# Optimization experiments

Measured on AMD Instinct MI355X. Metric: run time of the kernel, lower is better.

Reference implementation:

```python
import jax, jax.numpy as jnp
import numpy as np

N_HEADS = 16
THETA = 10000.0

def rotate_half(x):
    x1, x2 = jnp.split(x, 2, axis=-1)
    return jnp.concatenate((-x2, x1), axis=-1)

def setup_inputs() -> dict:
    key = jax.random.key(0)
    k1, k2, k3 = jax.random.split(key, 3)
    B, T, C = 4, 2048, 2048
    x = jax.random.normal(k1, (B, T, C), dtype=jnp.float32)
    # torch Linear weights: y = x @ W.T
    wqkv = jax.random.normal(k2, (3 * C, C), dtype=jnp.float32) * (1.0 / np.sqrt(C))
    w_out = jax.random.normal(k3, (C, C), dtype=jnp.float32) * (1.0 / np.sqrt(C))
    return {"x": x, "wqkv": wqkv, "w_out": w_out}

def reference(x, wqkv, w_out):
    B, T, C = x.shape
    H = N_HEADS
    hd = C // H
    scale = 1.0 / np.sqrt(hd)

    qkv = x @ wqkv.T                               # [B, T, 3C]
    q, k, v = jnp.split(qkv, 3, axis=-1)
    q = q.reshape(B, T, H, hd).transpose(0, 2, 1, 3)  # [B, H, T, hd]
    k = k.reshape(B, T, H, hd).transpose(0, 2, 1, 3)
    v = v.reshape(B, T, H, hd).transpose(0, 2, 1, 3)

    # rotary embedding (kv_len == T, no cache)
    inv_freq = 1.0 / (THETA ** (jnp.arange(0, hd, 2, dtype=jnp.float32) / hd))
    t = jnp.arange(T, dtype=jnp.float32)
    freqs = jnp.einsum("i,j->ij", t, inv_freq)     # [T, hd/2]
    emb = jnp.concatenate((freqs, freqs), axis=-1) # [T, hd]
    cos = jnp.cos(emb)[None, None, :, :]
    sin = jnp.sin(emb)[None, None, :, :]
    q = q * cos + rotate_half(q) * sin
    k = k * cos + rotate_half(k) * sin

    scores = jnp.einsum("bhqd,bhkd->bhqk", q, k) * scale
    causal = jnp.triu(jnp.ones((T, T), dtype=bool), k=1)
    scores = jnp.where(causal[None, None], -jnp.inf, scores)
    attn = jax.nn.softmax(scores, axis=-1)
    out = jnp.einsum("bhqk,bhkd->bhqd", attn, v)   # [B, H, T, hd]
    out = out.transpose(0, 2, 1, 3).reshape(B, T, C)
    output = out @ w_out.T
    return (output, k, v)
```

## Files before the change

### kernel.cpp

```cpp
#include <hip/hip_runtime.h>

#define B_ 4
#define T_ 2048
#define C_ 2048
#define H_ 16
#define HD_ 128
#define BT_ (B_*T_)
#define N3_ (3*C_)

typedef unsigned short u16;
typedef unsigned int u32;
using short8 = __attribute__((ext_vector_type(8))) short;
using f32x4  = __attribute__((ext_vector_type(4))) float;

__device__ __forceinline__ u16 f2bf(float f) {
  union { float f; u32 u; } v; v.f = f;
  u32 r = v.u + 0x7FFFu + ((v.u >> 16) & 1u);
  return (u16)(r >> 16);
}
__device__ __forceinline__ float bf2f(u16 u) {
  union { u32 u; float f; } v; v.u = ((u32)u) << 16;
  return v.f;
}
__device__ __forceinline__ void gload_lds16(const void* g, void* l) {
  __builtin_amdgcn_global_load_lds((const __attribute__((address_space(1))) void*)g,
                                   (__attribute__((address_space(3))) void*)l, 16, 0, 0);
}

__global__ __launch_bounds__(256) void cast_f2b_kernel(const float* __restrict__ in,
                                                       u16* __restrict__ out, int n4) {
  int i = blockIdx.x * 256 + threadIdx.x;
  if (i >= n4) return;
  float4 v = ((const float4*)in)[i];
  ushort4 o;
  o.x = f2bf(v.x); o.y = f2bf(v.y); o.z = f2bf(v.z); o.w = f2bf(v.w);
  ((ushort4*)out)[i] = o;
}

__global__ __launch_bounds__(256) void rope_table_kernel(float* __restrict__ cosb,
                                                         float* __restrict__ sinb) {
  int i = blockIdx.x * 256 + threadIdx.x;
  int t = i >> 6, d = i & 63;
  float inv = powf(10000.0f, -(float)d / 64.0f);
  float ang = (float)t * inv;
  cosb[i] = cosf(ang);
  sinb[i] = sinf(ang);
}

__global__ __launch_bounds__(256) void rope_apply_kernel(const u16* __restrict__ qkv,
    const float* __restrict__ cosb, const float* __restrict__ sinb,
    u16* __restrict__ qb, u16* __restrict__ kbb,
    float* __restrict__ kout, float* __restrict__ vout) {
  int gid = blockIdx.x * 256 + threadIdx.x;
  int d = gid & 63;
  int h = (gid >> 6) & 15;
  int t = (gid >> 10) & 2047;
  int b = gid >> 21;
  const u16* row = qkv + (size_t)(b * T_ + t) * N3_;
  int base = h * HD_ + d;
  const float SCALE = 0.08838834764831845f;
  float q0 = bf2f(row[base]);
  float q1 = bf2f(row[base + 64]);
  float k0 = bf2f(row[C_ + base]);
  float k1 = bf2f(row[C_ + base + 64]);
  float v0 = bf2f(row[2*C_ + base]);
  float v1 = bf2f(row[2*C_ + base + 64]);
  float c = cosb[t * 64 + d], s = sinb[t * 64 + d];
  size_t o = ((size_t)((b * H_ + h) * T_ + t)) * HD_ + d;
  qb[o]        = f2bf((q0 * c - q1 * s) * SCALE);
  qb[o + 64]   = f2bf((q1 * c + q0 * s) * SCALE);
  float kr0 = k0 * c - k1 * s;
  float kr1 = k1 * c + k0 * s;
  kout[o]      = kr0;
  kout[o + 64] = kr1;
  kbb[o]       = f2bf(kr0);
  kbb[o + 64]  = f2bf(kr1);
  vout[o]      = v0;
  vout[o + 64] = v1;
}

__global__ __launch_bounds__(256) void vt_kernel(const u16* __restrict__ qkvb,
                                                 u16* __restrict__ vtb) {
  __shared__ u16 tile[64][72];
  int bid = blockIdx.x;
  int dh = bid & 1, tt = (bid >> 1) & 31, bh = bid >> 6;
  int b = bh >> 4, h = bh & 15;
  int tid = threadIdx.x;
  int tr = tid >> 2, tc = tid & 3;
  const u16* src = qkvb + (size_t)(b*T_ + tt*64 + tr) * N3_ + 2*C_ + h*HD_ + dh*64 + tc*16;
  short8 v0 = *(const short8*)src;
  short8 v1 = *(const short8*)(src + 8);
  #pragma unroll
  for (int j = 0; j < 8; ++j) {
    tile[tr][tc*16 + j]     = (u16)v0[j];
    tile[tr][tc*16 + 8 + j] = (u16)v1[j];
  }
  __syncthreads();
  int dr = tid >> 2, c2 = tid & 3;
  short8 o0, o1;
  #pragma unroll
  for (int j = 0; j < 8; ++j) {
    o0[j] = (short)tile[c2*16 + j][dr];
    o1[j] = (short)tile[c2*16 + 8 + j][dr];
  }
  u16* dst = vtb + ((size_t)bh * HD_ + dh*64 + dr) * T_ + tt*64 + c2*16;
  *(short8*)dst = o0;
  *(short8*)(dst + 8) = o1;
}

template<int OUT_BF16>
__global__ __launch_bounds__(512, 2) void gemm3p_kernel(const u16* __restrict__ A,
    const u16* __restrict__ Bw, void* __restrict__ Cout, int M, int N, int K, int ntx) {
  extern __shared__ u16 ldsx[];
  int lin = blockIdx.x;
  int x = lin & 7, q = lin >> 3;
  int j = q & 31, rr = q >> 5;
  int rid = rr * 8 + x;
  int rgn = ntx >> 2;
  int rmr = rid / rgn, rnr = rid - rmr * rgn;
  int mtile = rmr * 8 + (j >> 2);
  int ntile = rnr * 4 + (j & 3);
  int tid = threadIdx.x, w = tid >> 6, l = tid & 63;
  int lr = l & 15, lg = l >> 4;
  int wr = w >> 2, wc = w & 3;
  const u16* Abase = A + (size_t)mtile * 256 * K;
  const u16* Bbase = Bw + (size_t)ntile * 256 * K;

  int srow[2], scol[2], sdst[2];
  #pragma unroll
  for (int jj = 0; jj < 2; ++jj) {
    int s = jj*512 + tid;
    srow[jj] = (s >> 6)*8 + (s & 7);
    scol[jj] = ((s >> 3) & 7) * 8;
    sdst[jj] = s * 8;
  }
  int arow[8], brow[4];
  #pragma unroll
  for (int mi = 0; mi < 8; ++mi) {
    int rho = mi*16 + lr;
    arow[mi] = (rho >> 3)*512 + (rho & 7)*8 + lg*64;
  }
  #pragma unroll
  for (int nj = 0; nj < 4; ++nj) {
    int rho = (wc & 1)*64 + nj*16 + lr;
    brow[nj] = (rho >> 3)*512 + (rho & 7)*8 + lg*64;
  }
  const int haOff = (2 + wr) * 8192;
  const int hbOff = (wc >> 1) * 8192;

  auto stageB = [&](int Tp) {
    u16* dst = ldsx + (Tp & 1) * 32768;
    const u16* g = Bbase + Tp * 64;
    #pragma unroll
    for (int jj = 0; jj < 2; ++jj)
      gload_lds16(g + (size_t)srow[jj] * K + scol[jj], dst + sdst[jj]);
    #pragma unroll
    for (int jj = 0; jj < 2; ++jj)
      gload_lds16(g + (size_t)(128 + srow[jj]) * K + scol[jj], dst + 8192 + sdst[jj]);
  };
  auto stageA = [&](int Tp) {
    u16* dst = ldsx + (Tp & 1) * 32768 + 16384;
    const u16* g = Abase + Tp * 64;
    #pragma unroll
    for (int jj = 0; jj < 2; ++jj)
      gload_lds16(g + (size_t)srow[jj] * K + scol[jj], dst + sdst[jj]);
    #pragma unroll
    for (int jj = 0; jj < 2; ++jj)
      gload_lds16(g + (size_t)(128 + srow[jj]) * K + scol[jj], dst + 8192 + sdst[jj]);
  };

  short8 am03[4][2], am47[4][2], bn01[2][2], bn23[2][2];
  auto readQ0 = [&](int T) {
    const u16* base = ldsx + (T & 1) * 32768;
    #pragma unroll
    for (int i = 0; i < 4; ++i)
      #pragma unroll
      for (int kk = 0; kk < 2; ++kk)
        am03[i][kk] = *(const short8*)(base + haOff + arow[i] + kk*256);
    #pragma unroll
    for (int jj = 0; jj < 2; ++jj)
      #pragma unroll
      for (int kk = 0; kk < 2; ++kk)
        bn01[jj][kk] = *(const short8*)(base + hbOff + brow[jj] + kk*256);
  };

  f32x4 acc[8][4];
  #pragma unroll
  for (int mi = 0; mi < 8; ++mi)
    #pragma unroll
    for (int n = 0; n < 4; ++n) acc[mi][n] = (f32x4){0.f,0.f,0.f,0.f};

  const int NT = K >> 6;
  stageB(0); stageA(0); stageB(1); stageA(1);
  asm volatile("s_waitcnt vmcnt(8)" ::: "memory");
  __builtin_amdgcn_sched_barrier(0);
  __builtin_amdgcn_s_barrier();
  readQ0(0);

  for (int T = 0; T < NT; ++T) {
    const u16* base = ldsx + (T & 1) * 32768;
    bool stg = (T + 2) < NT;
    #pragma unroll
    for (int jj = 0; jj < 2; ++jj)
      #pragma unroll
      for (int kk = 0; kk < 2; ++kk)
        bn23[jj][kk] = *(const short8*)(base + hbOff + brow[2+jj] + kk*256);
    __builtin_amdgcn_s_barrier();
    __builtin_amdgcn_s_setprio(1);
    #pragma unroll
    for (int i = 0; i < 4; ++i)
      #pragma unroll
      for (int jj = 0; jj < 2; ++jj)
        #pragma unroll
        for (int kk = 0; kk < 2; ++kk)
          acc[i][jj] = __builtin_amdgcn_mfma_f32_16x16x32_bf16(am03[i][kk], bn01[jj][kk], acc[i][jj], 0, 0, 0);
    __builtin_amdgcn_s_setprio(0);
    __builtin_amdgcn_s_barrier();
    if (stg) stageB(T + 2);
    #pragma unroll
    for (int i = 0; i < 4; ++i)
      #pragma unroll
      for (int kk = 0; kk < 2; ++kk)
        am47[i][kk] = *(const short8*)(base + haOff + arow[4+i] + kk*256);
    __builtin_amdgcn_s_barrier();
    __builtin_amdgcn_s_setprio(1);
    #pragma unroll
    for (int i = 0; i < 4; ++i)
      #pragma unroll
      for (int jj = 0; jj < 2; ++jj)
        #pragma unroll
        for (int kk = 0; kk < 2; ++kk)
          acc[i][2+jj] = __builtin_amdgcn_mfma_f32_16x16x32_bf16(am03[i][kk], bn23[jj][kk], acc[i][2+jj], 0, 0, 0);
    __builtin_amdgcn_s_setprio(0);
    __builtin_amdgcn_s_barrier();
    if (stg) {
      stageA(T + 2);
      asm volatile("s_waitcnt vmcnt(8)" ::: "memory");
    } else {
      asm volatile("s_waitcnt vmcnt(0)" ::: "memory");
    }
    __builtin_amdgcn_sched_barrier(0);
    __builtin_amdgcn_s_barrier();
    __builtin_amdgcn_s_setprio(1);
    #pragma unroll
    for (int i = 0; i < 4; ++i)
      #pragma unroll
      for (int jj = 0; jj < 2; ++jj)
        #pragma unroll
        for (int kk = 0; kk < 2; ++kk)
          acc[4+i][2+jj] = __builtin_amdgcn_mfma_f32_16x16x32_bf16(am47[i][kk], bn23[jj][kk], acc[4+i][2+jj], 0, 0, 0);
    #pragma unroll
    for (int i = 0; i < 4; ++i)
      #pragma unroll
      for (int jj = 0; jj < 2; ++jj)
        #pragma unroll
        for (int kk = 0; kk < 2; ++kk)
          acc[4+i][jj] = __builtin_amdgcn_mfma_f32_16x16x32_bf16(am47[i][kk], bn01[jj][kk], acc[4+i][jj], 0, 0, 0);
    __builtin_amdgcn_s_setprio(0);
    if (T + 1 < NT) readQ0(T + 1);
    __builtin_amdgcn_s_barrier();
  }
  #pragma unroll
  for (int mi = 0; mi < 8; ++mi)
    #pragma unroll
    for (int n = 0; n < 4; ++n)
      #pragma unroll
      for (int r = 0; r < 4; ++r) {
        int grow = mtile*256 + wr*128 + mi*16 + lg*4 + r;
        int gcol = ntile*256 + wc*64 + n*16 + lr;
        float v = acc[mi][n][r];
        if (OUT_BF16) ((u16*)Cout)[(size_t)grow * N + gcol] = f2bf(v);
        else          ((float*)Cout)[(size_t)grow * N + gcol] = v;
      }
}

struct TileSt {
  short8 aq[4];
  f32x4 oacc[8];
  float m_run[4];
  float l_run[4];
};

__device__ __forceinline__ void stage_kv(const u16* kpl, const u16* vpl, int kt,
                                         u16* Kd, u16* Vd, int w, int l) {
  const u16* kTile = kpl + (size_t)kt * 64 * HD_;
  int ktOff = kt * 64;
  #pragma unroll
  for (int j = 0; j < 4; ++j) {
    int s = (j*4 + w)*64 + l;
    int g = s ^ ((s >> 4) & 7);
    gload_lds16(kTile + (g >> 4)*HD_ + (g & 15)*8, (char*)Kd + (j*4 + w)*1024);
    int g2 = s ^ ((s >> 3) & 7);
    gload_lds16(vpl + (size_t)(g2 >> 3)*T_ + ktOff + (g2 & 7)*8, (char*)Vd + (j*4 + w)*1024);
  }
}

__device__ __forceinline__ void attn_tile(TileSt& st, const u16* Kl, const u16* Vl,
                                          char* Pw, bool diag, int lr, int lg, int w) {
  f32x4 s_acc[4];
  #pragma unroll
  for (int ct = 0; ct < 4; ++ct) s_acc[ct] = (f32x4){0.f, 0.f, 0.f, 0.f};
  __builtin_amdgcn_s_setprio(1);
  #pragma unroll
  for (int kg = 0; kg < 4; ++kg) {
    #pragma unroll
    for (int ct = 0; ct < 4; ++ct) {
      int krow = ct*16 + lr;
      int kbyte = (krow*256 + (kg*32 + lg*8)*2) ^ ((krow & 7) << 4);
      short8 bk = *(const short8*)((const char*)Kl + kbyte);
      s_acc[ct] = __builtin_amdgcn_mfma_f32_16x16x32_bf16(st.aq[kg], bk, s_acc[ct], 0, 0, 0);
    }
  }
  __builtin_amdgcn_s_setprio(0);
  float p[4][4];
  #pragma unroll
  for (int ct = 0; ct < 4; ++ct)
    #pragma unroll
    for (int r = 0; r < 4; ++r) {
      float sv = s_acc[ct][r];
      if (diag && (ct*16 + lr) > (w*16 + lg*4 + r)) sv = -INFINITY;
      p[ct][r] = sv;
    }
  float fac[4];
  #pragma unroll
  for (int r = 0; r < 4; ++r) {
    float mx = fmaxf(fmaxf(p[0][r], p[1][r]), fmaxf(p[2][r], p[3][r]));
    #pragma unroll
    for (int off = 1; off < 16; off <<= 1) mx = fmaxf(mx, __shfl_xor(mx, off));
    float mn = fmaxf(st.m_run[r], mx);
    fac[r] = __expf(st.m_run[r] - mn);
    st.m_run[r] = mn;
    float ls = 0.f;
    #pragma unroll
    for (int ct = 0; ct < 4; ++ct) { float pv = __expf(p[ct][r] - mn); p[ct][r] = pv; ls += pv; }
    #pragma unroll
    for (int off = 1; off < 16; off <<= 1) ls += __shfl_xor(ls, off);
    st.l_run[r] = st.l_run[r] * fac[r] + ls;
  }
  #pragma unroll
  for (int dt = 0; dt < 8; ++dt)
    #pragma unroll
    for (int r = 0; r < 4; ++r) st.oacc[dt][r] *= fac[r];
  #pragma unroll
  for (int ct = 0; ct < 4; ++ct)
    #pragma unroll
    for (int r = 0; r < 4; ++r) {
      int prow = lg*4 + r;
      int pb = (prow*128 + (ct*16 + lr)*2) ^ ((prow & 7) << 4);
      *(u16*)(Pw + pb) = f2bf(p[ct][r]);
    }
  asm volatile("s_waitcnt lgkmcnt(0)" ::: "memory");
  __builtin_amdgcn_sched_barrier(0);
  short8 pa[2];
  #pragma unroll
  for (int kk = 0; kk < 2; ++kk) {
    int pb = (lr*128 + (kk*32 + lg*8)*2) ^ ((lr & 7) << 4);
    pa[kk] = *(const short8*)(Pw + pb);
  }
  __builtin_amdgcn_s_setprio(1);
  #pragma unroll
  for (int dt = 0; dt < 8; ++dt) {
    #pragma unroll
    for (int kk = 0; kk < 2; ++kk) {
      int vrow = dt*16 + lr;
      int vbyte = (vrow*128 + (kk*32 + lg*8)*2) ^ ((vrow & 7) << 4);
      short8 bv = *(const short8*)((const char*)Vl + vbyte);
      st.oacc[dt] = __builtin_amdgcn_mfma_f32_16x16x32_bf16(pa[kk], bv, st.oacc[dt], 0, 0, 0);
    }
  }
  __builtin_amdgcn_s_setprio(0);
}

__device__ __forceinline__ void write_out(TileSt& st, u16* __restrict__ ao,
                                          int b, int h, int qbase, int lr, int lg, int w) {
  float invl[4];
  #pragma unroll
  for (int r = 0; r < 4; ++r) invl[r] = 1.0f / st.l_run[r];
  #pragma unroll
  for (int dt = 0; dt < 8; ++dt)
    #pragma unroll
    for (int r = 0; r < 4; ++r) {
      int t = qbase + w*16 + lg*4 + r;
      int col = h*HD_ + dt*16 + lr;
      ao[(size_t)(b * T_ + t) * C_ + col] = f2bf(st.oacc[dt][r] * invl[r]);
    }
}

__global__ __launch_bounds__(256, 2) void attn_kernel(const u16* __restrict__ qb,
    const u16* __restrict__ kb, const u16* __restrict__ vtb, u16* __restrict__ ao) {
  __shared__ u16 Kl[2][64 * 128];
  __shared__ u16 Vl[2][128 * 64];
  __shared__ u16 Pl[4][16 * 64];
  int bid0 = blockIdx.x;
  int bid = (bid0 & 7) * 128 + (bid0 >> 3);
  int bh = bid >> 4, pr = bid & 15;
  int lo = pr, hi = 31 - pr;
  int b = bh >> 4, h = bh & 15;
  int tid = threadIdx.x, w = tid >> 6, l = tid & 63;
  int lr = l & 15, lg = l >> 4;
  const u16* qptr = qb + (size_t)bh * T_ * HD_;
  const u16* kpl  = kb + (size_t)bh * T_ * HD_;
  const u16* vpl  = vtb + (size_t)bh * HD_ * T_;
  char* Pw = (char*)&Pl[w][0];

  TileSt stL, stH;
  #pragma unroll
  for (int kg = 0; kg < 4; ++kg) {
    stL.aq[kg] = *(const short8*)(qptr + (size_t)(lo*64 + w*16 + lr) * HD_ + kg*32 + lg*8);
    stH.aq[kg] = *(const short8*)(qptr + (size_t)(hi*64 + w*16 + lr) * HD_ + kg*32 + lg*8);
  }
  #pragma unroll
  for (int dt = 0; dt < 8; ++dt) {
    stL.oacc[dt] = (f32x4){0.f, 0.f, 0.f, 0.f};
    stH.oacc[dt] = (f32x4){0.f, 0.f, 0.f, 0.f};
  }
  #pragma unroll
  for (int r = 0; r < 4; ++r) {
    stL.m_run[r] = -INFINITY; stH.m_run[r] = -INFINITY;
    stL.l_run[r] = 0.f;       stH.l_run[r] = 0.f;
  }

  stage_kv(kpl, vpl, 0, &Kl[0][0], &Vl[0][0], w, l);
  __syncthreads();
  int cur = 0;
  for (int kt = 0; kt <= hi; ++kt) {
    if (kt < hi) stage_kv(kpl, vpl, kt + 1, &Kl[cur ^ 1][0], &Vl[cur ^ 1][0], w, l);
    attn_tile(stH, &Kl[cur][0], &Vl[cur][0], Pw, kt == hi, lr, lg, w);
    if (kt <= lo) attn_tile(stL, &Kl[cur][0], &Vl[cur][0], Pw, kt == lo, lr, lg, w);
    __syncthreads();
    cur ^= 1;
  }
  write_out(stH, ao, b, h, hi*64, lr, lg, w);
  write_out(stL, ao, b, h, lo*64, lr, lg, w);
}

extern "C" void kernel_launch(void* const* d_in, const int* in_sizes, int n_in,
                              void* d_out, int out_size, void* d_ws, size_t ws_size,
                              hipStream_t stream) {
  const float* x     = (const float*)d_in[0];
  const float* wqkv  = (const float*)d_in[1];
  const float* w_out = (const float*)d_in[2];
  float* out = (float*)d_out;

  char* ws = (char*)d_ws;
  size_t off = 0;
  u16* xb    = (u16*)(ws + off); off += (size_t)BT_ * C_ * 2;
  u16* wqkvb = (u16*)(ws + off); off += (size_t)N3_ * C_ * 2;
  u16* woutb = (u16*)(ws + off); off += (size_t)C_ * C_ * 2;
  u16* qkvb  = (u16*)(ws + off); off += (size_t)BT_ * N3_ * 2;
  u16* qbf   = (u16*)(ws + off); off += (size_t)BT_ * C_ * 2;
  u16* aob   = (u16*)(ws + off); off += (size_t)BT_ * C_ * 2;
  u16* kbb   = (u16*)(ws + off); off += (size_t)BT_ * C_ * 2;
  u16* vtb   = (u16*)(ws + off); off += (size_t)BT_ * C_ * 2;
  float* cosb = (float*)(ws + off); off += (size_t)T_ * 64 * 4;
  float* sinb = (float*)(ws + off); off += (size_t)T_ * 64 * 4;

  float* kout = out + (size_t)BT_ * C_;
  float* vout = out + 2 * (size_t)BT_ * C_;

  hipFuncSetAttribute((const void*)gemm3p_kernel<1>,
                      hipFuncAttributeMaxDynamicSharedMemorySize, 131072);
  hipFuncSetAttribute((const void*)gemm3p_kernel<0>,
                      hipFuncAttributeMaxDynamicSharedMemorySize, 131072);

  cast_f2b_kernel<<<(BT_*C_/4)/256, 256, 0, stream>>>(x, xb, BT_*C_/4);
  cast_f2b_kernel<<<(N3_*C_/4)/256, 256, 0, stream>>>(wqkv, wqkvb, N3_*C_/4);
  cast_f2b_kernel<<<(C_*C_/4)/256, 256, 0, stream>>>(w_out, woutb, C_*C_/4);
  rope_table_kernel<<<(T_*64)/256, 256, 0, stream>>>(cosb, sinb);
  gemm3p_kernel<1><<<(N3_/256)*(BT_/256), 512, 131072, stream>>>(xb, wqkvb, qkvb, BT_, N3_, C_, N3_/256);
  rope_apply_kernel<<<(B_*T_*H_*64)/256, 256, 0, stream>>>(qkvb, cosb, sinb, qbf, kbb, kout, vout);
  vt_kernel<<<B_*H_*(T_/64)*2, 256, 0, stream>>>(qkvb, vtb);
  attn_kernel<<<B_*H_*16, 256, 0, stream>>>(qbf, kbb, vtb, aob);
  gemm3p_kernel<0><<<(C_/256)*(BT_/256), 512, 131072, stream>>>(aob, woutb, out, BT_, C_, C_, C_/256);
}
```

Before: 573.3 us.

## Fuse RoPE, head-major scatter and V transpose into QKV GEMM epilogue

The QKV projection GEMM epilogue now stages each 128-row half of its output tile in LDS as bf16. From there it applies rotary embedding and writes q/k in head-major layout, writes fp32 k/v outputs, and writes transposed V directly. This removes the intermediate qkv buffer round-trip and two separate kernels (rope_apply and vt). The cost is a longer epilogue with extra barriers and LDS traffic inside the GEMM, plus strided transposed-V stores.

```diff
diff --git a/kernel.cpp b/kernel.cpp
--- a/kernel.cpp
+++ b/kernel.cpp
@@ -47,70 +47,12 @@
   sinb[i] = sinf(ang);
 }
 
-__global__ __launch_bounds__(256) void rope_apply_kernel(const u16* __restrict__ qkv,
-    const float* __restrict__ cosb, const float* __restrict__ sinb,
-    u16* __restrict__ qb, u16* __restrict__ kbb,
-    float* __restrict__ kout, float* __restrict__ vout) {
-  int gid = blockIdx.x * 256 + threadIdx.x;
-  int d = gid & 63;
-  int h = (gid >> 6) & 15;
-  int t = (gid >> 10) & 2047;
-  int b = gid >> 21;
-  const u16* row = qkv + (size_t)(b * T_ + t) * N3_;
-  int base = h * HD_ + d;
-  const float SCALE = 0.08838834764831845f;
-  float q0 = bf2f(row[base]);
-  float q1 = bf2f(row[base + 64]);
-  float k0 = bf2f(row[C_ + base]);
-  float k1 = bf2f(row[C_ + base + 64]);
-  float v0 = bf2f(row[2*C_ + base]);
-  float v1 = bf2f(row[2*C_ + base + 64]);
-  float c = cosb[t * 64 + d], s = sinb[t * 64 + d];
-  size_t o = ((size_t)((b * H_ + h) * T_ + t)) * HD_ + d;
-  qb[o]        = f2bf((q0 * c - q1 * s) * SCALE);
-  qb[o + 64]   = f2bf((q1 * c + q0 * s) * SCALE);
-  float kr0 = k0 * c - k1 * s;
-  float kr1 = k1 * c + k0 * s;
-  kout[o]      = kr0;
-  kout[o + 64] = kr1;
-  kbb[o]       = f2bf(kr0);
-  kbb[o + 64]  = f2bf(kr1);
-  vout[o]      = v0;
-  vout[o + 64] = v1;
-}
-
-__global__ __launch_bounds__(256) void vt_kernel(const u16* __restrict__ qkvb,
-                                                 u16* __restrict__ vtb) {
-  __shared__ u16 tile[64][72];
-  int bid = blockIdx.x;
-  int dh = bid & 1, tt = (bid >> 1) & 31, bh = bid >> 6;
-  int b = bh >> 4, h = bh & 15;
-  int tid = threadIdx.x;
-  int tr = tid >> 2, tc = tid & 3;
-  const u16* src = qkvb + (size_t)(b*T_ + tt*64 + tr) * N3_ + 2*C_ + h*HD_ + dh*64 + tc*16;
-  short8 v0 = *(const short8*)src;
-  short8 v1 = *(const short8*)(src + 8);
-  #pragma unroll
-  for (int j = 0; j < 8; ++j) {
-    tile[tr][tc*16 + j]     = (u16)v0[j];
-    tile[tr][tc*16 + 8 + j] = (u16)v1[j];
-  }
-  __syncthreads();
-  int dr = tid >> 2, c2 = tid & 3;
-  short8 o0, o1;
-  #pragma unroll
-  for (int j = 0; j < 8; ++j) {
-    o0[j] = (short)tile[c2*16 + j][dr];
-    o1[j] = (short)tile[c2*16 + 8 + j][dr];
-  }
-  u16* dst = vtb + ((size_t)bh * HD_ + dh*64 + dr) * T_ + tt*64 + c2*16;
-  *(short8*)dst = o0;
-  *(short8*)(dst + 8) = o1;
-}
-
-template<int OUT_BF16>
+template<int MODE>
 __global__ __launch_bounds__(512, 2) void gemm3p_kernel(const u16* __restrict__ A,
-    const u16* __restrict__ Bw, void* __restrict__ Cout, int M, int N, int K, int ntx) {
+    const u16* __restrict__ Bw, void* __restrict__ Cout, int M, int N, int K, int ntx,
+    u16* __restrict__ qb, u16* __restrict__ kbb, float* __restrict__ kout,
+    float* __restrict__ vout, u16* __restrict__ vtb,
+    const float* __restrict__ cosb, const float* __restrict__ sinb) {
   extern __shared__ u16 ldsx[];
   int lin = blockIdx.x;
   int x = lin & 7, q = lin >> 3;
@@ -260,18 +202,111 @@
     if (T + 1 < NT) readQ0(T + 1);
     __builtin_amdgcn_s_barrier();
   }
-  #pragma unroll
-  for (int mi = 0; mi < 8; ++mi)
-    #pragma unroll
-    for (int n = 0; n < 4; ++n)
-      #pragma unroll
-      for (int r = 0; r < 4; ++r) {
-        int grow = mtile*256 + wr*128 + mi*16 + lg*4 + r;
-        int gcol = ntile*256 + wc*64 + n*16 + lr;
-        float v = acc[mi][n][r];
-        if (OUT_BF16) ((u16*)Cout)[(size_t)grow * N + gcol] = f2bf(v);
-        else          ((float*)Cout)[(size_t)grow * N + gcol] = v;
+
+  if (MODE == 0) {
+    #pragma unroll
+    for (int mi = 0; mi < 8; ++mi)
+      #pragma unroll
+      for (int n = 0; n < 4; ++n)
+        #pragma unroll
+        for (int r = 0; r < 4; ++r) {
+          int grow = mtile*256 + wr*128 + mi*16 + lg*4 + r;
+          int gcol = ntile*256 + wc*64 + n*16 + lr;
+          ((float*)Cout)[(size_t)grow * N + gcol] = acc[mi][n][r];
+        }
+  } else {
+    const float SCALE = 0.08838834764831845f;
+    u16* eld = ldsx;
+    int btype = ntile >> 3;
+    int colg0 = ntile * 256;
+    #pragma unroll 1
+    for (int h = 0; h < 2; ++h) {
+      __builtin_amdgcn_s_barrier();
+      if (wr == h) {
+        #pragma unroll
+        for (int mi = 0; mi < 8; ++mi)
+          #pragma unroll
+          for (int n = 0; n < 4; ++n)
+            #pragma unroll
+            for (int r = 0; r < 4; ++r) {
+              int row = mi*16 + lg*4 + r;
+              int col = wc*64 + n*16 + lr;
+              eld[row*256 + col] = f2bf(acc[mi][n][r]);
+            }
       }
+      __builtin_amdgcn_s_barrier();
+      int grow0 = mtile*256 + h*128;
+      if (btype < 2) {
+        #pragma unroll 1
+        for (int ps = 0; ps < 8; ++ps) {
+          int ch = ps*512 + tid;
+          int row = ch >> 5, c8 = (ch & 31) * 8;
+          int grow = grow0 + row;
+          int t = grow & 2047, bb = grow >> 11;
+          int cq = colg0 + c8 - btype*2048;
+          int hh = cq >> 7;
+          float vals[8];
+          #pragma unroll
+          for (int e = 0; e < 8; ++e) {
+            int c = c8 + e;
+            int dloc = c & 127;
+            int dd = dloc & 63;
+            float cs = cosb[t*64 + dd], sn = sinb[t*64 + dd];
+            float x0 = bf2f(eld[row*256 + c]);
+            float x1 = bf2f(eld[row*256 + (c ^ 64)]);
+            vals[e] = (dloc < 64) ? (x0*cs - x1*sn) : (x0*cs + x1*sn);
+          }
+          size_t obase = ((size_t)(bb*16 + hh)*2048 + t)*128 + (cq & 127);
+          if (btype == 0) {
+            short8 pk;
+            #pragma unroll
+            for (int e = 0; e < 8; ++e) pk[e] = (short)f2bf(vals[e]*SCALE);
+            *(short8*)(qb + obase) = pk;
+          } else {
+            short8 pk;
+            #pragma unroll
+            for (int e = 0; e < 8; ++e) pk[e] = (short)f2bf(vals[e]);
+            *(short8*)(kbb + obase) = pk;
+            float4 f0 = {vals[0], vals[1], vals[2], vals[3]};
+            float4 f1 = {vals[4], vals[5], vals[6], vals[7]};
+            *(float4*)(kout + obase) = f0;
+            *(float4*)(kout + obase + 4) = f1;
+          }
+        }
+      } else {
+        #pragma unroll 1
+        for (int ps = 0; ps < 8; ++ps) {
+          int ch = ps*512 + tid;
+          int row = ch >> 5, c8 = (ch & 31) * 8;
+          int grow = grow0 + row;
+          int t = grow & 2047, bb = grow >> 11;
+          int cv = colg0 + c8 - 4096;
+          int hh = cv >> 7;
+          size_t obase = ((size_t)(bb*16 + hh)*2048 + t)*128 + (cv & 127);
+          float4 f0, f1;
+          #pragma unroll
+          for (int e = 0; e < 4; ++e) f0[e] = bf2f(eld[row*256 + c8 + e]);
+          #pragma unroll
+          for (int e = 0; e < 4; ++e) f1[e] = bf2f(eld[row*256 + c8 + 4 + e]);
+          *(float4*)(vout + obase) = f0;
+          *(float4*)(vout + obase + 4) = f1;
+        }
+        #pragma unroll 1
+        for (int ps = 0; ps < 8; ++ps) {
+          int ch = ps*512 + tid;
+          int c = ch >> 4, rg = (ch & 15) * 8;
+          int cv = colg0 + c - 4096;
+          int hh = cv >> 7, dd = cv & 127;
+          int grow = grow0 + rg;
+          int t0 = grow & 2047, bb = grow >> 11;
+          short8 pk;
+          #pragma unroll
+          for (int e = 0; e < 8; ++e) pk[e] = (short)eld[(rg + e)*256 + c];
+          *(short8*)(vtb + ((size_t)(bb*16 + hh)*128 + dd)*2048 + t0) = pk;
+        }
+      }
+    }
+  }
 }
 
 struct TileSt {
@@ -447,7 +482,6 @@
   u16* xb    = (u16*)(ws + off); off += (size_t)BT_ * C_ * 2;
   u16* wqkvb = (u16*)(ws + off); off += (size_t)N3_ * C_ * 2;
   u16* woutb = (u16*)(ws + off); off += (size_t)C_ * C_ * 2;
-  u16* qkvb  = (u16*)(ws + off); off += (size_t)BT_ * N3_ * 2;
   u16* qbf   = (u16*)(ws + off); off += (size_t)BT_ * C_ * 2;
   u16* aob   = (u16*)(ws + off); off += (size_t)BT_ * C_ * 2;
   u16* kbb   = (u16*)(ws + off); off += (size_t)BT_ * C_ * 2;
@@ -467,9 +501,11 @@
   cast_f2b_kernel<<<(N3_*C_/4)/256, 256, 0, stream>>>(wqkv, wqkvb, N3_*C_/4);
   cast_f2b_kernel<<<(C_*C_/4)/256, 256, 0, stream>>>(w_out, woutb, C_*C_/4);
   rope_table_kernel<<<(T_*64)/256, 256, 0, stream>>>(cosb, sinb);
-  gemm3p_kernel<1><<<(N3_/256)*(BT_/256), 512, 131072, stream>>>(xb, wqkvb, qkvb, BT_, N3_, C_, N3_/256);
-  rope_apply_kernel<<<(B_*T_*H_*64)/256, 256, 0, stream>>>(qkvb, cosb, sinb, qbf, kbb, kout, vout);
-  vt_kernel<<<B_*H_*(T_/64)*2, 256, 0, stream>>>(qkvb, vtb);
+  gemm3p_kernel<1><<<(N3_/256)*(BT_/256), 512, 131072, stream>>>(
+      xb, wqkvb, nullptr, BT_, N3_, C_, N3_/256,
+      qbf, kbb, kout, vout, vtb, cosb, sinb);
   attn_kernel<<<B_*H_*16, 256, 0, stream>>>(qbf, kbb, vtb, aob);
-  gemm3p_kernel<0><<<(C_/256)*(BT_/256), 512, 131072, stream>>>(aob, woutb, out, BT_, C_, C_, C_/256);
-}
+  gemm3p_kernel<0><<<(C_/256)*(BT_/256), 512, 131072, stream>>>(
+      aob, woutb, out, BT_, C_, C_, C_/256,
+      nullptr, nullptr, nullptr, nullptr, nullptr, nullptr, nullptr);
+}
```

Measured after the change: 642.0 us. 12.0% more time.
